# Kernel optimization log

Measured on AMD Instinct MI355X. Metric: run time of the kernel, lower is better.

## Reference

```python
import jax, jax.numpy as jnp
import numpy as np

B = 131072
HID = 256


def setup_inputs() -> dict:
    key = jax.random.key(0)
    ks = jax.random.split(key, 16)
    f32 = jnp.float32
    inp = {
        "theta_dot": jax.random.normal(ks[0], (B, 3), f32),
        "s_dot": jax.random.normal(ks[1], (B, 3), f32),
        "theta": jax.random.normal(ks[2], (B, 3), f32),
        "z": jax.random.normal(ks[3], (B, 1), f32),
        "s": jax.random.normal(ks[4], (B, 3), f32),
        "s_Ddot": jax.random.normal(ks[5], (B, 3), f32),
        "tau": jax.random.normal(ks[6], (B, 3), f32),
        # Lagrangian MLP (10 -> HID -> HID -> 1), tanh so 2nd derivs exist
        "LW1": jax.random.normal(ks[7], (10, HID), f32) / np.sqrt(10.0),
        "Lb1": jnp.zeros((HID,), f32),
        "LW2": jax.random.normal(ks[8], (HID, HID), f32) / np.sqrt(HID * 1.0),
        "Lb2": jnp.zeros((HID,), f32),
        "LW3": jax.random.normal(ks[9], (HID, 1), f32) / np.sqrt(HID * 1.0),
        "Lb3": jnp.zeros((1,), f32),
        # B_NN MLP (9 -> HID -> 3)
        "BW1": jax.random.normal(ks[10], (9, HID), f32) / np.sqrt(9.0),
        "Bb1": jnp.zeros((HID,), f32),
        "BW2": jax.random.normal(ks[11], (HID, 3), f32) / np.sqrt(HID * 1.0),
        "Bb2": jnp.zeros((3,), f32),
    }
    return inp


def reference(theta_dot, s_dot, theta, z, s, s_Ddot, tau,
              LW1, Lb1, LW2, Lb2, LW3, Lb3, BW1, Bb1, BW2, Bb2):
    def lagrangian(td, th, sd, zz):
        # single-sample scalar Lagrangian L(theta_dot, s_dot, theta, z)
        x = jnp.concatenate([td, sd, th, zz])  # (10,)
        h = jnp.tanh(x @ LW1 + Lb1)
        h = jnp.tanh(h @ LW2 + Lb2)
        return (h @ LW3 + Lb3)[0]

    g_td = jax.grad(lagrangian, argnums=0)  # dL/dtheta_dot : (3,)
    g_th = jax.grad(lagrangian, argnums=1)  # dL/dtheta     : (3,)

    def per_sample(td, sd, th, zz):
        H = jax.jacfwd(g_td, argnums=0)(td, th, sd, zz)   # d2L/dtd dtd (3,3)
        C = jax.jacfwd(g_th, argnums=0)(td, th, sd, zz)   # d2L/dth dtd (3,3)
        dth = g_th(td, th, sd, zz)                        # (3,)
        return H, C, dth

    H, C, dLdTheta = jax.vmap(per_sample)(theta_dot, s_dot, theta, z)

    # B_NN(theta, s, s_Ddot) -> (B, 3, 1)
    xb = jnp.concatenate([theta, s, s_Ddot], axis=-1)  # (B, 9)
    hb = jnp.tanh(xb @ BW1 + Bb1)
    Bout = (hb @ BW2 + Bb2)[..., None]

    rhs = (tau[..., None] + Bout + dLdTheta[..., None]
           - C @ theta_dot[..., None])                  # (B, 3, 1)
    return jnp.linalg.inv(H) @ rhs                      # (B, 3, 1)
```

## Files before the change

kernel.cpp:

```cpp
#include <hip/hip_runtime.h>

#define HID 256
#define SB  16

typedef float v2f __attribute__((ext_vector_type(2)));
typedef float v4f __attribute__((ext_vector_type(4)));
typedef int   i32x4 __attribute__((ext_vector_type(4)));
typedef int   i32x2 __attribute__((ext_vector_type(2)));

__device__ __forceinline__ float fast_tanh(float x) {
    float ax = __builtin_fabsf(x);
    float e  = __expf(2.0f * ax);
    float t  = 1.0f - 2.0f * __builtin_amdgcn_rcpf(e + 1.0f);
    return __builtin_copysignf(t, x);
}

__device__ __forceinline__ v2f pk_fma_lo(v2f a, v2f b, v2f c) {
    asm("v_pk_fma_f32 %0, %1, %2, %0 op_sel_hi:[1,0,1]" : "+v"(c) : "v"(a), "v"(b));
    return c;
}
__device__ __forceinline__ v2f pk_fma_hi(v2f a, v2f b, v2f c) {
    asm("v_pk_fma_f32 %0, %1, %2, %0 op_sel:[0,1,0] op_sel_hi:[1,1,1]" : "+v"(c) : "v"(a), "v"(b));
    return c;
}

__device__ __forceinline__ v2f red64(v2f v) {
#pragma unroll
    for (int m = 1; m < 64; m <<= 1) {
        v.x += __shfl_xor(v.x, m, 64);
        v.y += __shfl_xor(v.y, m, 64);
    }
    return v;
}

__device__ __forceinline__ float red_lq(float v) {
    v += __shfl_xor(v, 16, 64);
    v += __shfl_xor(v, 32, 64);
    return v;
}

__device__ __forceinline__ float hsum4(v4f v) { return (v.x + v.y) + (v.z + v.w); }

__device__ __forceinline__ void split3(float x, unsigned short& h, unsigned short& m, unsigned short& l) {
    unsigned u0 = __float_as_uint(x);
    unsigned short hh = (unsigned short)((u0 + 0x7FFFu + ((u0 >> 16) & 1u)) >> 16);
    float r1 = x - __uint_as_float((unsigned)hh << 16);
    unsigned u1 = __float_as_uint(r1);
    unsigned short mm = (unsigned short)((u1 + 0x7FFFu + ((u1 >> 16) & 1u)) >> 16);
    float r2 = r1 - __uint_as_float((unsigned)mm << 16);
    unsigned u2 = __float_as_uint(r2);
    unsigned short ll = (unsigned short)((u2 + 0x7FFFu + ((u2 >> 16) & 1u)) >> 16);
    h = hh; m = mm; l = ll;
}

__device__ __forceinline__ void mfma_acc(v4f& d, i32x4 a, i32x4 b) {
    asm("v_mfma_f32_16x16x32_bf16 %0, %1, %2, %0" : "+v"(d) : "v"(a), "v"(b));
}

__device__ __forceinline__ v4f mfma_safe(i32x4 a, i32x4 b) {
    v4f d = (v4f){0.0f, 0.0f, 0.0f, 0.0f};
    asm("s_nop 1\n\tv_mfma_f32_16x16x32_bf16 %0, %1, %2, %0\n\ts_nop 7\n\ts_nop 3"
        : "+v"(d) : "v"(a), "v"(b));
    return d;
}

__device__ __forceinline__ void mfma_read_fence() {
    asm volatile("s_nop 7\n\ts_nop 3" ::: "memory");
}

__device__ __forceinline__ int x1_off(int p, int j, int kb16) {
    int g = (kb16 ^ (j & 15) ^ ((j >> 4) << 2)) & 15;
    return p * 16384 + j * 256 + (g << 4);
}
__device__ __forceinline__ int x2_off(int p, int j2, int kb16) {
    int g = (kb16 ^ (j2 & 15) ^ ((j2 >> 4) << 3)) & 31;
    return p * 16384 + j2 * 512 + (g << 4);
}

#define ACC4(DST, SRC) \
    DST[0] = pk_fma_lo(SRC, wlo, DST[0]); \
    DST[1] = pk_fma_hi(SRC, wlo, DST[1]); \
    DST[2] = pk_fma_lo(SRC, whi, DST[2]); \
    DST[3] = pk_fma_hi(SRC, whi, DST[3]);

__global__ void build_planes(const float* __restrict__ LW2, unsigned short* __restrict__ P) {
    int t = blockIdx.x * 256 + threadIdx.x;
    int tensor = t >> 13;
    int pos = t & 8191;
    int l = pos & 63, ks = (pos >> 6) & 7, Mt = pos >> 9;
    int mrow = Mt * 16 + (l & 15);
    int kb = ks * 32 + ((l >> 4) << 3);
    unsigned short sh[3][8];
#pragma unroll
    for (int i = 0; i < 8; ++i) {
        float v = tensor ? LW2[mrow * HID + kb + i] : LW2[(kb + i) * HID + mrow];
        split3(v, sh[0][i], sh[1][i], sh[2][i]);
    }
#pragma unroll
    for (int p = 0; p < 3; ++p) {
        unsigned short* dst = P + (tensor * 3 + p) * 65536 + pos * 8;
#pragma unroll
        for (int i = 0; i < 8; ++i) dst[i] = sh[p][i];
    }
}

__launch_bounds__(512, 4)
__global__ void lnn_mfma(
    const float* __restrict__ g_td, const float* __restrict__ g_sd,
    const float* __restrict__ g_th, const float* __restrict__ g_z,
    const float* __restrict__ g_s,  const float* __restrict__ g_sdd,
    const float* __restrict__ g_tau,
    const float* __restrict__ LW1, const float* __restrict__ Lb1,
    const float* __restrict__ Lb2, const float* __restrict__ LW3,
    const float* __restrict__ BW1, const float* __restrict__ Bb1,
    const float* __restrict__ BW2, const float* __restrict__ Bb2,
    const unsigned short* __restrict__ PL,
    float* __restrict__ out)
{
    __shared__ __align__(16) unsigned char ldsX[49152];
    __shared__ __align__(16) float h1L[16 * 260];
    __shared__ __align__(16) float xs2[16][SB];
    __shared__ __align__(16) float redM[8][SB][18];
    __shared__ __align__(16) float red2[SB][3];

    const int tid = threadIdx.x;
    const int c   = tid & 63;
    const int r   = tid >> 6;
    const int l15 = c & 15;
    const int lq  = c >> 4;
    const int mt0 = r * 2;
    const int sg0 = blockIdx.x * SB;

    if (tid < SB * 3) {
        int s = tid / 3, m = tid - s * 3;
        xs2[m][s]      = g_td [(sg0 + s) * 3 + m];
        xs2[3 + m][s]  = g_sd [(sg0 + s) * 3 + m];
        xs2[6 + m][s]  = g_th [(sg0 + s) * 3 + m];
        xs2[10 + m][s] = g_s  [(sg0 + s) * 3 + m];
        xs2[13 + m][s] = g_sdd[(sg0 + s) * 3 + m];
    } else if (tid < SB * 4) {
        int s = tid - SB * 3;
        xs2[9][s] = g_z[sg0 + s];
    }
    __syncthreads();

    {
        int kk = tid & 255;
        int sbase = (tid >> 8) * 8;
        float a1[8];
#pragma unroll
        for (int e = 0; e < 8; ++e) a1[e] = 0.0f;
#pragma unroll
        for (int m = 0; m < 10; ++m) {
            float w = LW1[m * HID + kk];
#pragma unroll
            for (int e = 0; e < 8; ++e)
                a1[e] = __builtin_fmaf(xs2[m][sbase + e], w, a1[e]);
        }
        float bb = Lb1[kk];
#pragma unroll
        for (int e = 0; e < 8; ++e)
            h1L[(sbase + e) * 260 + kk] = fast_tanh(a1[e] + bb);
    }

    {
        const int k0 = c * 4;
        const int s0 = r * 2;
        v2f ab[4];
#pragma unroll
        for (int q = 0; q < 4; ++q) ab[q] = (v2f){0.0f, 0.0f};
#pragma unroll
        for (int m = 0; m < 9; ++m) {
            v4f w4v = *(const v4f*)(BW1 + m * HID + k0);
            v2f wlo = __builtin_shufflevector(w4v, w4v, 0, 1);
            v2f whi = __builtin_shufflevector(w4v, w4v, 2, 3);
            int xi = (m < 3) ? (6 + m) : (7 + m);
            v2f xmv = *(const v2f*)&xs2[xi][s0];
            ACC4(ab, xmv);
        }
        v4f bbv = *(const v4f*)(Bb1 + k0);
        v2f bp0 = (v2f){0,0}, bp1 = (v2f){0,0}, bp2 = (v2f){0,0};
#pragma unroll
        for (int q = 0; q < 4; ++q) {
            int k = k0 + q;
            v2f hb2; hb2.x = fast_tanh(ab[q].x + bbv[q]); hb2.y = fast_tanh(ab[q].y + bbv[q]);
            bp0 += hb2 * BW2[k * 3 + 0];
            bp1 += hb2 * BW2[k * 3 + 1];
            bp2 += hb2 * BW2[k * 3 + 2];
        }
        bp0 = red64(bp0); bp1 = red64(bp1); bp2 = red64(bp2);
        if (c == 0) {
            red2[s0][0] = bp0.x; red2[s0 + 1][0] = bp0.y;
            red2[s0][1] = bp1.x; red2[s0 + 1][1] = bp1.y;
            red2[s0][2] = bp2.x; red2[s0 + 1][2] = bp2.y;
        }
    }
    __syncthreads();

    v4f acc[2][4], alo[2][4];
#pragma unroll
    for (int m = 0; m < 2; ++m)
#pragma unroll
        for (int b = 0; b < 4; ++b) { acc[m][b] = (v4f){0,0,0,0}; alo[m][b] = (v4f){0,0,0,0}; }

    for (int half = 0; half < 2; ++half) {
        {
            int s = c & 15, f = c >> 4;
            int kb = half * 128 + r * 16;
            float vv[16];
#pragma unroll
            for (int qq = 0; qq < 4; ++qq) {
                v4f h4 = *(const v4f*)&h1L[s * 260 + kb + qq * 4];
                if (f == 0) {
#pragma unroll
                    for (int e = 0; e < 4; ++e) vv[qq * 4 + e] = h4[e];
                } else {
                    v4f wq = *(const v4f*)(LW1 + (f - 1) * HID + kb + qq * 4);
#pragma unroll
                    for (int e = 0; e < 4; ++e) vv[qq * 4 + e] = (1.0f - h4[e] * h4[e]) * wq[e];
                }
            }
            unsigned short sp[3][16];
#pragma unroll
            for (int e = 0; e < 16; ++e) split3(vv[e], sp[0][e], sp[1][e], sp[2][e]);
#pragma unroll
            for (int p = 0; p < 3; ++p)
#pragma unroll
                for (int bh = 0; bh < 2; ++bh) {
                    i32x4 pk;
#pragma unroll
                    for (int d = 0; d < 4; ++d)
                        pk[d] = (int)sp[p][bh * 8 + 2 * d] | ((int)sp[p][bh * 8 + 2 * d + 1] << 16);
                    *(i32x4*)(ldsX + x1_off(p, c, r * 2 + bh)) = pk;
                }
        }
        __syncthreads();
        for (int ksl = 0; ksl < 4; ++ksl) {
            int ksg = half * 4 + ksl;
            int kb16 = ksl * 4 + lq;
            const unsigned short* a0 = PL + mt0 * 4096 + ksg * 512 + c * 8;
            i32x4 Ah[2], Am[2], Al[2];
#pragma unroll
            for (int m = 0; m < 2; ++m) {
                Ah[m] = *(const i32x4*)(a0 + m * 4096);
                Am[m] = *(const i32x4*)(a0 + 65536 + m * 4096);
                Al[m] = *(const i32x4*)(a0 + 131072 + m * 4096);
            }
#pragma unroll
            for (int b = 0; b < 4; ++b) {
                i32x4 B = *(const i32x4*)(ldsX + x1_off(0, b * 16 + l15, kb16));
                acc[0][b] += mfma_safe(Ah[0], B);
                acc[1][b] += mfma_safe(Ah[1], B);
                mfma_acc(alo[0][b], Am[0], B); mfma_acc(alo[1][b], Am[1], B);
                mfma_acc(alo[0][b], Al[0], B); mfma_acc(alo[1][b], Al[1], B);
            }
#pragma unroll
            for (int b = 0; b < 4; ++b) {
                i32x4 B = *(const i32x4*)(ldsX + x1_off(1, b * 16 + l15, kb16));
                mfma_acc(alo[0][b], Ah[0], B); mfma_acc(alo[1][b], Ah[1], B);
                mfma_acc(alo[0][b], Am[0], B); mfma_acc(alo[1][b], Am[1], B);
            }
#pragma unroll
            for (int b = 0; b < 4; ++b) {
                i32x4 B = *(const i32x4*)(ldsX + x1_off(2, b * 16 + l15, kb16));
                mfma_acc(alo[0][b], Ah[0], B); mfma_acc(alo[1][b], Ah[1], B);
            }
        }
        __syncthreads();
    }
    mfma_read_fence();
#pragma unroll
    for (int m = 0; m < 2; ++m)
#pragma unroll
        for (int b = 0; b < 4; ++b) acc[m][b] += alo[m][b];

    float Hp[6] = {0, 0, 0, 0, 0, 0};
    const int sE = l15;
    const float td0s = xs2[0][sE], td1s = xs2[1][sE], td2s = xs2[2][sE];
#pragma unroll
    for (int m = 0; m < 2; ++m) {
        int nq = (mt0 + m) * 16 + lq * 4;
        v4f b2 = *(const v4f*)(Lb2 + nq);
        v4f w3 = *(const v4f*)(LW3 + nq);
        unsigned short sg[3][4], sd[3][4];
#pragma unroll
        for (int i = 0; i < 4; ++i) {
            float a2 = acc[m][0][i] + b2[i];
            float P0 = acc[m][1][i], P1 = acc[m][2][i], P2 = acc[m][3][i];
            float h2 = fast_tanh(a2);
            float t2 = 1.0f - h2 * h2;
            float g2 = t2 * w3[i];
            float m2 = -2.0f * h2 * g2;
            Hp[0] += m2 * P0 * P0; Hp[1] += m2 * P0 * P1; Hp[2] += m2 * P1 * P1;
            Hp[3] += m2 * P0 * P2; Hp[4] += m2 * P1 * P2; Hp[5] += m2 * P2 * P2;
            float pd = m2 * (P0 * td0s + P1 * td1s + P2 * td2s);
            split3(g2, sg[0][i], sg[1][i], sg[2][i]);
            split3(pd, sd[0][i], sd[1][i], sd[2][i]);
        }
        int kb16 = (mt0 + m) * 2 + (lq >> 1);
        int off8 = (lq & 1) * 8;
#pragma unroll
        for (int p = 0; p < 3; ++p) {
            i32x2 a, bpk;
            a[0]   = (int)sg[p][0] | ((int)sg[p][1] << 16);
            a[1]   = (int)sg[p][2] | ((int)sg[p][3] << 16);
            bpk[0] = (int)sd[p][0] | ((int)sd[p][1] << 16);
            bpk[1] = (int)sd[p][2] | ((int)sd[p][3] << 16);
            *(i32x2*)(ldsX + x2_off(p, sE, kb16) + off8)      = a;
            *(i32x2*)(ldsX + x2_off(p, 16 + sE, kb16) + off8) = bpk;
        }
    }
#pragma unroll
    for (int j = 0; j < 6; ++j) {
        float v = red_lq(Hp[j]);
        if (lq == 0) redM[r][sE][j] = v;
    }
    __syncthreads();

    v4f acc2[2][2], alo2[2][2];
#pragma unroll
    for (int m = 0; m < 2; ++m)
#pragma unroll
        for (int b = 0; b < 2; ++b) { acc2[m][b] = (v4f){0,0,0,0}; alo2[m][b] = (v4f){0,0,0,0}; }

    for (int ks = 0; ks < 8; ++ks) {
        int kb16 = ks * 4 + lq;
        const unsigned short* a0 = PL + 196608 + mt0 * 4096 + ks * 512 + c * 8;
        i32x4 Ah[2], Am[2], Al[2];
#pragma unroll
        for (int m = 0; m < 2; ++m) {
            Ah[m] = *(const i32x4*)(a0 + m * 4096);
            Am[m] = *(const i32x4*)(a0 + 65536 + m * 4096);
            Al[m] = *(const i32x4*)(a0 + 131072 + m * 4096);
        }
#pragma unroll
        for (int b = 0; b < 2; ++b) {
            i32x4 B = *(const i32x4*)(ldsX + x2_off(0, b * 16 + l15, kb16));
            acc2[0][b] += mfma_safe(Ah[0], B);
            acc2[1][b] += mfma_safe(Ah[1], B);
            mfma_acc(alo2[0][b], Am[0], B); mfma_acc(alo2[1][b], Am[1], B);
            mfma_acc(alo2[0][b], Al[0], B); mfma_acc(alo2[1][b], Al[1], B);
        }
#pragma unroll
        for (int b = 0; b < 2; ++b) {
            i32x4 B = *(const i32x4*)(ldsX + x2_off(1, b * 16 + l15, kb16));
            mfma_acc(alo2[0][b], Ah[0], B); mfma_acc(alo2[1][b], Ah[1], B);
            mfma_acc(alo2[0][b], Am[0], B); mfma_acc(alo2[1][b], Am[1], B);
        }
#pragma unroll
        for (int b = 0; b < 2; ++b) {
            i32x4 B = *(const i32x4*)(ldsX + x2_off(2, b * 16 + l15, kb16));
            mfma_acc(alo2[0][b], Ah[0], B); mfma_acc(alo2[1][b], Ah[1], B);
        }
    }
    mfma_read_fence();
#pragma unroll
    for (int m = 0; m < 2; ++m)
#pragma unroll
        for (int b = 0; b < 2; ++b) acc2[m][b] += alo2[m][b];

    {
        v4f dl0 = (v4f){0,0,0,0}, dl1 = dl0, dl2 = dl0;
        v4f ct0 = dl0, ct1 = dl0, ct2 = dl0;
        v4f hd[6];
#pragma unroll
        for (int j = 0; j < 6; ++j) hd[j] = (v4f){0,0,0,0};
#pragma unroll
        for (int m = 0; m < 2; ++m) {
            int kq = (mt0 + m) * 16 + lq * 4;
            v4f U = acc2[m][0];
            v4f W = acc2[m][1];
            v4f h1 = *(const v4f*)&h1L[sE * 260 + kq];
            v4f wd0 = *(const v4f*)(LW1 + 0 * HID + kq);
            v4f wd1 = *(const v4f*)(LW1 + 1 * HID + kq);
            v4f wd2 = *(const v4f*)(LW1 + 2 * HID + kq);
            v4f wt0 = *(const v4f*)(LW1 + 6 * HID + kq);
            v4f wt1 = *(const v4f*)(LW1 + 7 * HID + kq);
            v4f wt2 = *(const v4f*)(LW1 + 8 * HID + kq);
            v4f t1 = 1.0f - h1 * h1;
            v4f g1 = U * t1;
            dl0 += g1 * wt0; dl1 += g1 * wt1; dl2 += g1 * wt2;
            v4f cf = -2.0f * U * h1 * t1;
            v4f wdtd = td0s * wd0 + td1s * wd1 + td2s * wd2;
            v4f ct = t1 * W + cf * wdtd;
            ct0 += ct * wt0; ct1 += ct * wt1; ct2 += ct * wt2;
            hd[0] += cf * wd0 * wd0; hd[1] += cf * wd0 * wd1; hd[2] += cf * wd1 * wd1;
            hd[3] += cf * wd0 * wd2; hd[4] += cf * wd1 * wd2; hd[5] += cf * wd2 * wd2;
        }
        float vals[12];
        vals[0] = hsum4(dl0); vals[1] = hsum4(dl1); vals[2] = hsum4(dl2);
        vals[3] = hsum4(ct0); vals[4] = hsum4(ct1); vals[5] = hsum4(ct2);
#pragma unroll
        for (int j = 0; j < 6; ++j) vals[6 + j] = hsum4(hd[j]);
#pragma unroll
        for (int j = 0; j < 12; ++j) {
            float v = red_lq(vals[j]);
            if (lq == 0) redM[r][sE][6 + j] = v;
        }
    }
    __syncthreads();

    if (tid < SB) {
        int s = tid;
        int gs = sg0 + s;
        double Ha = 0, Hb = 0, Hd = 0, Hc = 0, He = 0, Hf = 0;
        double dL0 = 0, dL1 = 0, dL2 = 0, ct0 = 0, ct1 = 0, ct2 = 0;
#pragma unroll
        for (int w = 0; w < 8; ++w) {
            Ha += (double)redM[w][s][0] + (double)redM[w][s][12];
            Hb += (double)redM[w][s][1] + (double)redM[w][s][13];
            Hd += (double)redM[w][s][2] + (double)redM[w][s][14];
            Hc += (double)redM[w][s][3] + (double)redM[w][s][15];
            He += (double)redM[w][s][4] + (double)redM[w][s][16];
            Hf += (double)redM[w][s][5] + (double)redM[w][s][17];
            dL0 += redM[w][s][6]; dL1 += redM[w][s][7]; dL2 += redM[w][s][8];
            ct0 += redM[w][s][9]; ct1 += redM[w][s][10]; ct2 += redM[w][s][11];
        }
        double rhs[3];
        rhs[0] = (double)g_tau[gs * 3 + 0] + (double)red2[s][0] + (double)Bb2[0] + dL0 - ct0;
        rhs[1] = (double)g_tau[gs * 3 + 1] + (double)red2[s][1] + (double)Bb2[1] + dL1 - ct1;
        rhs[2] = (double)g_tau[gs * 3 + 2] + (double)red2[s][2] + (double)Bb2[2] + dL2 - ct2;
        double I00 = Hd * Hf - He * He;
        double I01 = Hc * He - Hb * Hf;
        double I02 = Hb * He - Hc * Hd;
        double I11 = Ha * Hf - Hc * Hc;
        double I12 = Hb * Hc - Ha * He;
        double I22 = Ha * Hd - Hb * Hb;
        double det = Ha * I00 + Hb * I01 + Hc * I02;
        double inv = 1.0 / det;
        out[gs * 3 + 0] = (float)((I00 * rhs[0] + I01 * rhs[1] + I02 * rhs[2]) * inv);
        out[gs * 3 + 1] = (float)((I01 * rhs[0] + I11 * rhs[1] + I12 * rhs[2]) * inv);
        out[gs * 3 + 2] = (float)((I02 * rhs[0] + I12 * rhs[1] + I22 * rhs[2]) * inv);
    }
}

__global__ void transpose256(const float* __restrict__ in, float* __restrict__ outT) {
    __shared__ float tile[32][33];
    const int tid = threadIdx.x;
    const int bx = blockIdx.x & 7;
    const int by = blockIdx.x >> 3;
    const int tx = tid & 31, ty = tid >> 5;
#pragma unroll
    for (int yy = ty; yy < 32; yy += 8)
        tile[yy][tx] = in[(by * 32 + yy) * HID + bx * 32 + tx];
    __syncthreads();
#pragma unroll
    for (int yy = ty; yy < 32; yy += 8)
        outT[(bx * 32 + yy) * HID + by * 32 + tx] = tile[tx][yy];
}

__device__ __forceinline__ v2f pk_mul_lo(v2f a, v2f b) {
    v2f d;
    asm("v_pk_mul_f32 %0, %1, %2 op_sel_hi:[1,0]" : "=v"(d) : "v"(a), "v"(b));
    return d;
}
__device__ __forceinline__ v2f pk_mul_hi(v2f a, v2f b) {
    v2f d;
    asm("v_pk_mul_f32 %0, %1, %2 op_sel:[0,1] op_sel_hi:[1,1]" : "=v"(d) : "v"(a), "v"(b));
    return d;
}

__launch_bounds__(256, 4)
__global__ void lnn_valu(
    const float* __restrict__ g_td, const float* __restrict__ g_sd,
    const float* __restrict__ g_th, const float* __restrict__ g_z,
    const float* __restrict__ g_s,  const float* __restrict__ g_sdd,
    const float* __restrict__ g_tau,
    const float* __restrict__ LW1, const float* __restrict__ Lb1,
    const float* __restrict__ LW2, const float* __restrict__ Lb2,
    const float* __restrict__ LW3,
    const float* __restrict__ BW1, const float* __restrict__ Bb1,
    const float* __restrict__ BW2, const float* __restrict__ Bb2,
    const float* __restrict__ W2T,
    float* __restrict__ out)
{
    __shared__ __align__(16) float ldsP[HID * 32];
    __shared__ __align__(16) float xs2[16][8];
    __shared__ __align__(16) float red[8][16];

    const int tid = threadIdx.x;
    const int c   = tid & 63;
    const int r   = tid >> 6;
    const int k0  = c * 4;
    const int s0  = r * 2;
    const int sg0 = blockIdx.x * 8;
    const int o1  = r * 8;
    const int o2  = r * 4;
    const int sw1 = (c & 3) << 3;
    const int sw2 = (c & 3) << 2;

    if (tid < 24) {
        int s = tid / 3, m = tid - s * 3;
        xs2[m][s]      = g_td [(sg0 + s) * 3 + m];
        xs2[3 + m][s]  = g_sd [(sg0 + s) * 3 + m];
        xs2[6 + m][s]  = g_th [(sg0 + s) * 3 + m];
        xs2[10 + m][s] = g_s  [(sg0 + s) * 3 + m];
        xs2[13 + m][s] = g_sdd[(sg0 + s) * 3 + m];
    } else if (tid < 32) {
        int s = tid - 24;
        xs2[9][s] = g_z[sg0 + s];
    }
    __syncthreads();

    float h1r[2][4];
    {
        v2f a1[4];
#pragma unroll
        for (int q = 0; q < 4; ++q) a1[q] = (v2f){0.0f, 0.0f};
#pragma unroll
        for (int m = 0; m < 10; ++m) {
            v4f w4 = *(const v4f*)(LW1 + m * HID + k0);
            v2f wlo = __builtin_shufflevector(w4, w4, 0, 1);
            v2f whi = __builtin_shufflevector(w4, w4, 2, 3);
            v2f xmv = *(const v2f*)&xs2[m][s0];
            ACC4(a1, xmv);
        }
        v4f bb  = *(const v4f*)(Lb1 + k0);
        v4f wd0 = *(const v4f*)(LW1 + 0 * HID + k0);
        v4f wd1 = *(const v4f*)(LW1 + 1 * HID + k0);
        v4f wd2 = *(const v4f*)(LW1 + 2 * HID + k0);
#pragma unroll
        for (int q = 0; q < 4; ++q) {
            float hx = fast_tanh(a1[q].x + bb[q]);
            float hy = fast_tanh(a1[q].y + bb[q]);
            h1r[0][q] = hx; h1r[1][q] = hy;
            float tx = 1.0f - hx * hx, ty = 1.0f - hy * hy;
            int rb = (k0 + q) * 32 + (o1 ^ sw1);
            *(v4f*)&ldsP[rb]     = (v4f){ hx, hy, tx * wd0[q], ty * wd0[q] };
            *(v4f*)&ldsP[rb + 4] = (v4f){ tx * wd1[q], ty * wd1[q], tx * wd2[q], ty * wd2[q] };
        }
    }

    {
        v2f ab[4];
#pragma unroll
        for (int q = 0; q < 4; ++q) ab[q] = (v2f){0.0f, 0.0f};
#pragma unroll
        for (int m = 0; m < 9; ++m) {
            v4f w4 = *(const v4f*)(BW1 + m * HID + k0);
            v2f wlo = __builtin_shufflevector(w4, w4, 0, 1);
            v2f whi = __builtin_shufflevector(w4, w4, 2, 3);
            int xi = (m < 3) ? (6 + m) : (7 + m);
            v2f xmv = *(const v2f*)&xs2[xi][s0];
            ACC4(ab, xmv);
        }
        v4f bbv = *(const v4f*)(Bb1 + k0);
        v2f bp0 = (v2f){0,0}, bp1 = (v2f){0,0}, bp2 = (v2f){0,0};
#pragma unroll
        for (int q = 0; q < 4; ++q) {
            int k = k0 + q;
            v2f hb; hb.x = fast_tanh(ab[q].x + bbv[q]); hb.y = fast_tanh(ab[q].y + bbv[q]);
            bp0 += hb * BW2[k * 3 + 0];
            bp1 += hb * BW2[k * 3 + 1];
            bp2 += hb * BW2[k * 3 + 2];
        }
        bp0 = red64(bp0); bp1 = red64(bp1); bp2 = red64(bp2);
        if (c == 0) {
            red[s0][12] = bp0.x; red[s0 + 1][12] = bp0.y;
            red[s0][13] = bp1.x; red[s0 + 1][13] = bp1.y;
            red[s0][14] = bp2.x; red[s0 + 1][14] = bp2.y;
        }
    }
    __syncthreads();

    v2f acc[4][4];
#pragma unroll
    for (int f = 0; f < 4; ++f)
#pragma unroll
        for (int q = 0; q < 4; ++q) acc[f][q] = (v2f){0.0f, 0.0f};

    for (int n0 = 0; n0 < HID; n0 += 4) {
        const float* prow = &ldsP[n0 * 32 + (o1 ^ (((n0 >> 2) & 3) << 3))];
        const float* wrow = LW2 + n0 * HID + k0;
#pragma unroll
        for (int j = 0; j < 4; ++j) {
            v4f pA = *(const v4f*)(prow + j * 32);
            v4f pB = *(const v4f*)(prow + j * 32 + 4);
            v4f w4 = *(const v4f*)(wrow + j * HID);
            v2f wlo = __builtin_shufflevector(w4, w4, 0, 1);
            v2f whi = __builtin_shufflevector(w4, w4, 2, 3);
            v2f hv = __builtin_shufflevector(pA, pA, 0, 1);
            v2f i1 = __builtin_shufflevector(pA, pA, 2, 3);
            v2f i2 = __builtin_shufflevector(pB, pB, 0, 1);
            v2f i3 = __builtin_shufflevector(pB, pB, 2, 3);
            ACC4(acc[0], hv);
            ACC4(acc[1], i1);
            ACC4(acc[2], i2);
            ACC4(acc[3], i3);
        }
    }
    __syncthreads();

    v2f Hp[6];
#pragma unroll
    for (int i = 0; i < 6; ++i) Hp[i] = (v2f){0.0f, 0.0f};
    const v2f td0v = *(const v2f*)&xs2[0][s0];
    const v2f td1v = *(const v2f*)&xs2[1][s0];
    const v2f td2v = *(const v2f*)&xs2[2][s0];
    {
        v4f b2v = *(const v4f*)(Lb2 + k0);
        v4f w3v = *(const v4f*)(LW3 + k0);
#pragma unroll
        for (int q = 0; q < 4; ++q) {
            v2f a2 = acc[0][q] + b2v[q];
            v2f h2; h2.x = fast_tanh(a2.x); h2.y = fast_tanh(a2.y);
            v2f t2 = 1.0f - h2 * h2;
            v2f g2 = t2 * w3v[q];
            v2f m2 = -2.0f * h2 * g2;
            v2f P0 = acc[1][q], P1 = acc[2][q], P2 = acc[3][q];
            v2f m2P0 = m2 * P0, m2P1 = m2 * P1;
            Hp[0] += m2P0 * P0;
            Hp[1] += m2P0 * P1;
            Hp[2] += m2P1 * P1;
            Hp[3] += m2P0 * P2;
            Hp[4] += m2P1 * P2;
            Hp[5] += m2 * P2 * P2;
            v2f ptd = td0v * P0 + td1v * P1 + td2v * P2;
            v2f pd  = m2 * ptd;
            *(v4f*)&ldsP[(k0 + q) * 32 + (o2 ^ sw2)] = (v4f){ g2.x, g2.y, pd.x, pd.y };
        }
    }
    __syncthreads();

#pragma unroll
    for (int f = 0; f < 2; ++f)
#pragma unroll
        for (int q = 0; q < 4; ++q) acc[f][q] = (v2f){0.0f, 0.0f};

    for (int n0 = 0; n0 < HID; n0 += 4) {
        const float* prow = &ldsP[n0 * 32 + (o2 ^ (((n0 >> 2) & 3) << 2))];
        const float* wrow = W2T + n0 * HID + k0;
#pragma unroll
        for (int j = 0; j < 4; ++j) {
            v4f p  = *(const v4f*)(prow + j * 32);
            v4f w4 = *(const v4f*)(wrow + j * HID);
            v2f wlo = __builtin_shufflevector(w4, w4, 0, 1);
            v2f whi = __builtin_shufflevector(w4, w4, 2, 3);
            v2f g2v = __builtin_shufflevector(p, p, 0, 1);
            v2f pdv = __builtin_shufflevector(p, p, 2, 3);
            ACC4(acc[0], g2v);
            ACC4(acc[1], pdv);
        }
    }

    v2f dLp[3], ctp[3];
#pragma unroll
    for (int i = 0; i < 3; ++i) { dLp[i] = (v2f){0,0}; ctp[i] = (v2f){0,0}; }
    {
        v4f wd0 = *(const v4f*)(LW1 + 0 * HID + k0);
        v4f wd1 = *(const v4f*)(LW1 + 1 * HID + k0);
        v4f wd2 = *(const v4f*)(LW1 + 2 * HID + k0);
        v4f wt0 = *(const v4f*)(LW1 + 6 * HID + k0);
        v4f wt1 = *(const v4f*)(LW1 + 7 * HID + k0);
        v4f wt2 = *(const v4f*)(LW1 + 8 * HID + k0);
#pragma unroll
        for (int q = 0; q < 4; ++q) {
            v2f h1; h1.x = h1r[0][q]; h1.y = h1r[1][q];
            v2f t1 = 1.0f - h1 * h1;
            v2f u  = acc[0][q];
            v2f w  = acc[1][q];
            v2f g1 = u * t1;
            dLp[0] += g1 * wt0[q]; dLp[1] += g1 * wt1[q]; dLp[2] += g1 * wt2[q];
            v2f cf = -2.0f * u * h1 * t1;
            v2f wdtd = td0v * wd0[q] + td1v * wd1[q] + td2v * wd2[q];
            v2f ct = t1 * w + cf * wdtd;
            ctp[0] += ct * wt0[q]; ctp[1] += ct * wt1[q]; ctp[2] += ct * wt2[q];
            float w00 = wd0[q] * wd0[q], w01 = wd0[q] * wd1[q], w11 = wd1[q] * wd1[q];
            float w02 = wd0[q] * wd2[q], w12 = wd1[q] * wd2[q], w22 = wd2[q] * wd2[q];
            Hp[0] += cf * w00; Hp[1] += cf * w01; Hp[2] += cf * w11;
            Hp[3] += cf * w02; Hp[4] += cf * w12; Hp[5] += cf * w22;
        }
    }

#pragma unroll
    for (int i = 0; i < 6; ++i) {
        v2f v = red64(Hp[i]);
        if (c == 0) { red[s0][i] = v.x; red[s0 + 1][i] = v.y; }
    }
#pragma unroll
    for (int i = 0; i < 3; ++i) {
        v2f v = red64(dLp[i]);
        if (c == 0) { red[s0][6 + i] = v.x; red[s0 + 1][6 + i] = v.y; }
    }
#pragma unroll
    for (int i = 0; i < 3; ++i) {
        v2f v = red64(ctp[i]);
        if (c == 0) { red[s0][9 + i] = v.x; red[s0 + 1][9 + i] = v.y; }
    }
    __syncthreads();

    if (tid < 8) {
        int s = tid;
        int gs = sg0 + s;
        double Ha = red[s][0], Hb = red[s][1], Hd = red[s][2];
        double Hc = red[s][3], He = red[s][4], Hf = red[s][5];
        double rhs[3];
#pragma unroll
        for (int i = 0; i < 3; ++i) {
            rhs[i] = (double)g_tau[gs * 3 + i] + (double)red[s][12 + i] + (double)Bb2[i]
                   + (double)red[s][6 + i]
                   - (double)red[s][9 + i];
        }
        double I00 = Hd * Hf - He * He;
        double I01 = Hc * He - Hb * Hf;
        double I02 = Hb * He - Hc * Hd;
        double I11 = Ha * Hf - Hc * Hc;
        double I12 = Hb * Hc - Ha * He;
        double I22 = Ha * Hd - Hb * Hb;
        double det = Ha * I00 + Hb * I01 + Hc * I02;
        double inv = 1.0 / det;
        out[gs * 3 + 0] = (float)((I00 * rhs[0] + I01 * rhs[1] + I02 * rhs[2]) * inv);
        out[gs * 3 + 1] = (float)((I01 * rhs[0] + I11 * rhs[1] + I12 * rhs[2]) * inv);
        out[gs * 3 + 2] = (float)((I02 * rhs[0] + I12 * rhs[1] + I22 * rhs[2]) * inv);
    }
}

extern "C" void kernel_launch(void* const* d_in, const int* in_sizes, int n_in,
                              void* d_out, int out_size, void* d_ws, size_t ws_size,
                              hipStream_t stream) {
    const float* td  = (const float*)d_in[0];
    const float* sd  = (const float*)d_in[1];
    const float* th  = (const float*)d_in[2];
    const float* z   = (const float*)d_in[3];
    const float* s_  = (const float*)d_in[4];
    const float* sdd = (const float*)d_in[5];
    const float* tau = (const float*)d_in[6];
    const float* LW1 = (const float*)d_in[7];
    const float* Lb1 = (const float*)d_in[8];
    const float* LW2 = (const float*)d_in[9];
    const float* Lb2 = (const float*)d_in[10];
    const float* LW3 = (const float*)d_in[11];
    const float* BW1 = (const float*)d_in[13];
    const float* Bb1 = (const float*)d_in[14];
    const float* BW2 = (const float*)d_in[15];
    const float* Bb2 = (const float*)d_in[16];
    float* outp = (float*)d_out;

    const int Btot = in_sizes[0] / 3;

    if (ws_size >= 6u * 65536u * 2u) {
        unsigned short* planes = (unsigned short*)d_ws;
        build_planes<<<dim3(64), dim3(256), 0, stream>>>(LW2, planes);
        const int nblk = Btot / SB;
        lnn_mfma<<<dim3(nblk), dim3(512), 0, stream>>>(
            td, sd, th, z, s_, sdd, tau, LW1, Lb1, Lb2, LW3,
            BW1, Bb1, BW2, Bb2, planes, outp);
    } else {
        float* W2T = (float*)d_ws;
        transpose256<<<dim3(64), dim3(256), 0, stream>>>(LW2, W2T);
        const int nblk = Btot / 8;
        lnn_valu<<<dim3(nblk), dim3(256), 0, stream>>>(
            td, sd, th, z, s_, sdd, tau, LW1, Lb1, LW2, Lb2, LW3,
            BW1, Bb1, BW2, Bb2, W2T, outp);
    }
}
```

Measured before the change: 627.2 us.

## Batch hi-product MFMA accumulation over two k-steps to remove per-MFMA nop stalls

```diff
diff --git a/kernel.cpp b/kernel.cpp
--- a/kernel.cpp
+++ b/kernel.cpp
@@ -57,9 +57,9 @@
     asm("v_mfma_f32_16x16x32_bf16 %0, %1, %2, %0" : "+v"(d) : "v"(a), "v"(b));
 }
 
-__device__ __forceinline__ v4f mfma_safe(i32x4 a, i32x4 b) {
+__device__ __forceinline__ v4f mfma_start(i32x4 a, i32x4 b) {
     v4f d = (v4f){0.0f, 0.0f, 0.0f, 0.0f};
-    asm("s_nop 1\n\tv_mfma_f32_16x16x32_bf16 %0, %1, %2, %0\n\ts_nop 7\n\ts_nop 3"
+    asm("s_nop 1\n\tv_mfma_f32_16x16x32_bf16 %0, %1, %2, %0"
         : "+v"(d) : "v"(a), "v"(b));
     return d;
 }
@@ -104,7 +104,7 @@
     }
 }
 
-__launch_bounds__(512, 4)
+__launch_bounds__(512, 2)
 __global__ void lnn_mfma(
     const float* __restrict__ g_td, const float* __restrict__ g_sd,
     const float* __restrict__ g_th, const float* __restrict__ g_z,
@@ -235,40 +235,57 @@
                 }
         }
         __syncthreads();
-        for (int ksl = 0; ksl < 4; ++ksl) {
-            int ksg = half * 4 + ksl;
-            int kb16 = ksl * 4 + lq;
-            const unsigned short* a0 = PL + mt0 * 4096 + ksg * 512 + c * 8;
-            i32x4 Ah[2], Am[2], Al[2];
-#pragma unroll
-            for (int m = 0; m < 2; ++m) {
-                Ah[m] = *(const i32x4*)(a0 + m * 4096);
-                Am[m] = *(const i32x4*)(a0 + 65536 + m * 4096);
-                Al[m] = *(const i32x4*)(a0 + 131072 + m * 4096);
+        for (int ks2 = 0; ks2 < 2; ++ks2) {
+            v4f ahh[2][4];
+#pragma unroll
+            for (int kk = 0; kk < 2; ++kk) {
+                int ksl = ks2 * 2 + kk;
+                int ksg = half * 4 + ksl;
+                int kb16 = ksl * 4 + lq;
+                const unsigned short* a0 = PL + mt0 * 4096 + ksg * 512 + c * 8;
+                i32x4 Ah[2], Am[2], Al[2];
+#pragma unroll
+                for (int m = 0; m < 2; ++m) {
+                    Ah[m] = *(const i32x4*)(a0 + m * 4096);
+                    Am[m] = *(const i32x4*)(a0 + 65536 + m * 4096);
+                    Al[m] = *(const i32x4*)(a0 + 131072 + m * 4096);
+                }
+#pragma unroll
+                for (int b = 0; b < 4; ++b) {
+                    i32x4 B = *(const i32x4*)(ldsX + x1_off(0, b * 16 + l15, kb16));
+                    if (kk == 0) {
+                        ahh[0][b] = mfma_start(Ah[0], B);
+                        ahh[1][b] = mfma_start(Ah[1], B);
+                    } else {
+                        mfma_acc(ahh[0][b], Ah[0], B);
+                        mfma_acc(ahh[1][b], Ah[1], B);
+                    }
+                    mfma_acc(alo[0][b], Am[0], B); mfma_acc(alo[1][b], Am[1], B);
+                    mfma_acc(alo[0][b], Al[0], B); mfma_acc(alo[1][b], Al[1], B);
+                }
+#pragma unroll
+                for (int b = 0; b < 4; ++b) {
+                    i32x4 B = *(const i32x4*)(ldsX + x1_off(1, b * 16 + l15, kb16));
+                    mfma_acc(alo[0][b], Ah[0], B); mfma_acc(alo[1][b], Ah[1], B);
+                    mfma_acc(alo[0][b], Am[0], B); mfma_acc(alo[1][b], Am[1], B);
+                }
+#pragma unroll
+                for (int b = 0; b < 4; ++b) {
+                    i32x4 B = *(const i32x4*)(ldsX + x1_off(2, b * 16 + l15, kb16));
+                    mfma_acc(alo[0][b], Ah[0], B); mfma_acc(alo[1][b], Ah[1], B);
+                }
             }
-#pragma unroll
-            for (int b = 0; b < 4; ++b) {
-                i32x4 B = *(const i32x4*)(ldsX + x1_off(0, b * 16 + l15, kb16));
-                acc[0][b] += mfma_safe(Ah[0], B);
-                acc[1][b] += mfma_safe(Ah[1], B);
-                mfma_acc(alo[0][b], Am[0], B); mfma_acc(alo[1][b], Am[1], B);
-                mfma_acc(alo[0][b], Al[0], B); mfma_acc(alo[1][b], Al[1], B);
-            }
-#pragma unroll
-            for (int b = 0; b < 4; ++b) {
-                i32x4 B = *(const i32x4*)(ldsX + x1_off(1, b * 16 + l15, kb16));
-                mfma_acc(alo[0][b], Ah[0], B); mfma_acc(alo[1][b], Ah[1], B);
-                mfma_acc(alo[0][b], Am[0], B); mfma_acc(alo[1][b], Am[1], B);
-            }
-#pragma unroll
-            for (int b = 0; b < 4; ++b) {
-                i32x4 B = *(const i32x4*)(ldsX + x1_off(2, b * 16 + l15, kb16));
-                mfma_acc(alo[0][b], Ah[0], B); mfma_acc(alo[1][b], Ah[1], B);
-            }
+            mfma_read_fence();
+            __builtin_amdgcn_sched_barrier(0);
+#pragma unroll
+            for (int m = 0; m < 2; ++m)
+#pragma unroll
+                for (int b = 0; b < 4; ++b) acc[m][b] += ahh[m][b];
         }
         __syncthreads();
     }
     mfma_read_fence();
+    __builtin_amdgcn_sched_barrier(0);
 #pragma unroll
     for (int m = 0; m < 2; ++m)
 #pragma unroll
@@ -323,37 +340,54 @@
 #pragma unroll
         for (int b = 0; b < 2; ++b) { acc2[m][b] = (v4f){0,0,0,0}; alo2[m][b] = (v4f){0,0,0,0}; }
 
-    for (int ks = 0; ks < 8; ++ks) {
-        int kb16 = ks * 4 + lq;
-        const unsigned short* a0 = PL + 196608 + mt0 * 4096 + ks * 512 + c * 8;
-        i32x4 Ah[2], Am[2], Al[2];
-#pragma unroll
-        for (int m = 0; m < 2; ++m) {
-            Ah[m] = *(const i32x4*)(a0 + m * 4096);
-            Am[m] = *(const i32x4*)(a0 + 65536 + m * 4096);
-            Al[m] = *(const i32x4*)(a0 + 131072 + m * 4096);
-        }
-#pragma unroll
-        for (int b = 0; b < 2; ++b) {
-            i32x4 B = *(const i32x4*)(ldsX + x2_off(0, b * 16 + l15, kb16));
-            acc2[0][b] += mfma_safe(Ah[0], B);
-            acc2[1][b] += mfma_safe(Ah[1], B);
-            mfma_acc(alo2[0][b], Am[0], B); mfma_acc(alo2[1][b], Am[1], B);
-            mfma_acc(alo2[0][b], Al[0], B); mfma_acc(alo2[1][b], Al[1], B);
-        }
-#pragma unroll
-        for (int b = 0; b < 2; ++b) {
-            i32x4 B = *(const i32x4*)(ldsX + x2_off(1, b * 16 + l15, kb16));
-            mfma_acc(alo2[0][b], Ah[0], B); mfma_acc(alo2[1][b], Ah[1], B);
-            mfma_acc(alo2[0][b], Am[0], B); mfma_acc(alo2[1][b], Am[1], B);
-        }
-#pragma unroll
-        for (int b = 0; b < 2; ++b) {
-            i32x4 B = *(const i32x4*)(ldsX + x2_off(2, b * 16 + l15, kb16));
-            mfma_acc(alo2[0][b], Ah[0], B); mfma_acc(alo2[1][b], Ah[1], B);
-        }
+    for (int ks2 = 0; ks2 < 4; ++ks2) {
+        v4f ahh2[2][2];
+#pragma unroll
+        for (int kk = 0; kk < 2; ++kk) {
+            int ks = ks2 * 2 + kk;
+            int kb16 = ks * 4 + lq;
+            const unsigned short* a0 = PL + 196608 + mt0 * 4096 + ks * 512 + c * 8;
+            i32x4 Ah[2], Am[2], Al[2];
+#pragma unroll
+            for (int m = 0; m < 2; ++m) {
+                Ah[m] = *(const i32x4*)(a0 + m * 4096);
+                Am[m] = *(const i32x4*)(a0 + 65536 + m * 4096);
+                Al[m] = *(const i32x4*)(a0 + 131072 + m * 4096);
+            }
+#pragma unroll
+            for (int b = 0; b < 2; ++b) {
+                i32x4 B = *(const i32x4*)(ldsX + x2_off(0, b * 16 + l15, kb16));
+                if (kk == 0) {
+                    ahh2[0][b] = mfma_start(Ah[0], B);
+                    ahh2[1][b] = mfma_start(Ah[1], B);
+                } else {
+                    mfma_acc(ahh2[0][b], Ah[0], B);
+                    mfma_acc(ahh2[1][b], Ah[1], B);
+                }
+                mfma_acc(alo2[0][b], Am[0], B); mfma_acc(alo2[1][b], Am[1], B);
+                mfma_acc(alo2[0][b], Al[0], B); mfma_acc(alo2[1][b], Al[1], B);
+            }
+#pragma unroll
+            for (int b = 0; b < 2; ++b) {
+                i32x4 B = *(const i32x4*)(ldsX + x2_off(1, b * 16 + l15, kb16));
+                mfma_acc(alo2[0][b], Ah[0], B); mfma_acc(alo2[1][b], Ah[1], B);
+                mfma_acc(alo2[0][b], Am[0], B); mfma_acc(alo2[1][b], Am[1], B);
+            }
+#pragma unroll
+            for (int b = 0; b < 2; ++b) {
+                i32x4 B = *(const i32x4*)(ldsX + x2_off(2, b * 16 + l15, kb16));
+                mfma_acc(alo2[0][b], Ah[0], B); mfma_acc(alo2[1][b], Ah[1], B);
+            }
+        }
+        mfma_read_fence();
+        __builtin_amdgcn_sched_barrier(0);
+#pragma unroll
+        for (int m = 0; m < 2; ++m)
+#pragma unroll
+            for (int b = 0; b < 2; ++b) acc2[m][b] += ahh2[m][b];
     }
     mfma_read_fence();
+    __builtin_amdgcn_sched_barrier(0);
 #pragma unroll
     for (int m = 0; m < 2; ++m)
 #pragma unroll
```

After: 690.2 us. 1.1x slower.
